# Optimization experiments

Measured on AMD Instinct MI355X. Metric: run time of the kernel, lower is better.

The kernel has to match this reference:

```python
import jax, jax.numpy as jnp
import numpy as np

# tcnn HashGrid config from ntc_conf
L = 16            # n_levels
T = 1 << 15       # 2**log2_hashmap_size entries per level
F = 4             # n_features_per_level
BASE = 16.0       # base_resolution
N_PTS = 1_000_000
PRIMES = jnp.array([1, 2654435761, 805459861], dtype=jnp.uint32)  # tcnn spatial hash primes
OFFS = np.array([[(c >> 2) & 1, (c >> 1) & 1, c & 1] for c in range(8)], dtype=np.uint32)  # 8 cube corners


def hash_encode(x, table):
    """Multi-resolution hash grid encoding. x: [N,3] in [0,1], table: [L,T,F] -> [N, L*F]."""
    N = x.shape[0]
    scales = BASE * (2.0 ** jnp.arange(L, dtype=jnp.float32))        # [L]
    pos = x[:, None, :] * scales[None, :, None]                      # [N,L,3]
    p0 = jnp.floor(pos)
    frac = pos - p0                                                  # trilinear weights source
    p0u = p0.astype(jnp.uint32)
    flat_table = table.reshape(L * T, F)
    level_off = (jnp.arange(L, dtype=jnp.uint32) * jnp.uint32(T))[None, :]  # [1,L]
    acc = jnp.zeros((N, L, F), dtype=table.dtype)
    for c in range(8):  # fixed 8 corners -> keeps peak memory at [N,L,F] per corner
        off = jnp.asarray(OFFS[c])                                   # [3] uint32
        corner = p0u + off                                           # [N,L,3]
        h = corner * PRIMES                                          # uint32 wraparound mul
        idx = (h[..., 0] ^ h[..., 1] ^ h[..., 2]) & jnp.uint32(T - 1)  # [N,L]
        feats = flat_table[(idx + level_off).astype(jnp.int32)]      # gather [N,L,F]
        w = jnp.prod(jnp.where(off.astype(bool), frac, 1.0 - frac), axis=-1)  # [N,L]
        acc = acc + w[..., None] * feats
    return acc.reshape(N, L * F)


def setup_inputs() -> dict:
    key = jax.random.key(0)
    k1, k2, k3, k4, k5 = jax.random.split(key, 5)
    xyz = jax.random.normal(k1, (N_PTS, 3), dtype=jnp.float32)
    xyz_bound_min = -jnp.ones((3,), dtype=jnp.float32)
    xyz_bound_max = jnp.ones((3,), dtype=jnp.float32)
    hash_table = jax.random.normal(k2, (L, T, F), dtype=jnp.float32) * 1e-2  # tcnn-style small init
    w0 = jax.random.normal(k3, (64, 64), dtype=jnp.float32) * (1.0 / 8.0)
    w1 = jax.random.normal(k4, (64, 64), dtype=jnp.float32) * (1.0 / 8.0)
    w2 = jax.random.normal(k5, (64, 8), dtype=jnp.float32) * (1.0 / 8.0)
    return {"xyz": xyz, "xyz_bound_min": xyz_bound_min, "xyz_bound_max": xyz_bound_max,
            "hash_table": hash_table, "w0": w0, "w1": w1, "w2": w2}


def reference(xyz, xyz_bound_min, xyz_bound_max, hash_table, w0, w1, w2):
    contracted = (xyz - xyz_bound_min) / (xyz_bound_max - xyz_bound_min)   # [N,3]
    mask = jnp.all((contracted >= 0.0) & (contracted <= 1.0), axis=1)      # [N]
    # Evaluate on all points (clamped) and mask the writes -- equivalent to the
    # original compaction (contracted[mask]) + scatter-back, jit-friendly shapes.
    xin = jnp.clip(contracted, 0.0, 1.0)
    enc = hash_encode(xin, hash_table)                                     # [N,64]
    h = jax.nn.relu(enc @ w0)
    h = jax.nn.relu(h @ w1)
    resi = h @ w2                                                          # [N,8]
    d_xyz = jnp.where(mask[:, None], resi[:, :3], 0.0)
    ident_rot = jnp.array([1.0, 0.0, 0.0, 0.0], dtype=resi.dtype)
    d_rot = jnp.where(mask[:, None], resi[:, 3:7], ident_rot)
    return mask, d_xyz, d_rot
```

## Files before the change

### kernel.cpp

```cpp
#include <hip/hip_runtime.h>
#include <hip/hip_bf16.h>


#define LVL 16
#define TSZ 32768
#define PR1 2654435761u
#define PR2 805459861u
#define SUBS 16
#define STRIDE (SUBS * 1024)

typedef __attribute__((ext_vector_type(8))) short bf16x8;
typedef __attribute__((ext_vector_type(4))) float f32x4;
typedef __attribute__((ext_vector_type(2))) float f32x2;
typedef __attribute__((ext_vector_type(4))) unsigned short u16x4;
typedef __attribute__((ext_vector_type(2))) unsigned int u32x2;
typedef long long i64;

__device__ __forceinline__ unsigned short f2bf(float f) {
    return __builtin_bit_cast(unsigned short, __float2bfloat16(f));
}

__device__ __forceinline__ unsigned f32x4_to_fp8x4(float f0, float f1, float f2, float f3) {
#if __has_builtin(__builtin_amdgcn_cvt_pk_fp8_f32)
    int u = 0;
    u = __builtin_amdgcn_cvt_pk_fp8_f32(f0, f1, u, false);
    u = __builtin_amdgcn_cvt_pk_fp8_f32(f2, f3, u, true);
    return (unsigned)u;
#else
    float ff[4] = { f0, f1, f2, f3 };
    unsigned u = 0;
    for (int k = 0; k < 4; ++k) {
        const float v = ff[k];
        const unsigned s = v < 0.f ? 1u : 0u;
        float av = fabsf(v);
        unsigned b;
        if (av < 6.103515625e-05f) {
            b = 0u;
        } else if (av < 0.015625f) {
            b = (unsigned)rintf(av * 512.f);
        } else {
            int e; float m = frexpf(av, &e);
            unsigned E = (unsigned)(e - 1 + 7);
            unsigned q = (unsigned)rintf(m * 16.f);
            if (q == 16u) { q = 8u; ++E; }
            b = (E << 3) | (q - 8u);
        }
        u |= ((s << 7) | b) << (8 * k);
    }
    return u;
#endif
}

__device__ __forceinline__ unsigned char f32_to_fp8(float v) {
    return (unsigned char)(f32x4_to_fp8x4(v, v, v, v) & 0xffu);
}

__device__ __forceinline__ void fp8x4_to_2f32x2(unsigned r, f32x2& lo, f32x2& hi) {
#if __has_builtin(__builtin_amdgcn_cvt_pk_f32_fp8)
    lo = __builtin_amdgcn_cvt_pk_f32_fp8((int)r, false);
    hi = __builtin_amdgcn_cvt_pk_f32_fp8((int)r, true);
#else
    float f[4];
#pragma unroll
    for (int k = 0; k < 4; ++k) {
        const unsigned b = (r >> (8 * k)) & 0xffu;
        const unsigned s = b >> 7, em = b & 0x7fu, e = em >> 3, m = em & 7u;
        float v;
        if (e) v = __builtin_bit_cast(float, ((e + 120u) << 23) | (m << 20));
        else   v = (float)m * 0.001953125f;
        f[k] = s ? -v : v;
    }
    lo = (f32x2){ f[0], f[1] };
    hi = (f32x2){ f[2], f[3] };
#endif
}

__global__ __launch_bounds__(1024) void k_enc(
    const float* __restrict__ xyz, const float* __restrict__ bmin, const float* __restrict__ bmax,
    const float* __restrict__ table, float* __restrict__ out,
    unsigned* __restrict__ enc, int N, int Npad,
    const float* __restrict__ w0, const float* __restrict__ w1,
    const float* __restrict__ w2, char* __restrict__ wbase)
{
    __shared__ unsigned tabL[TSZ];

    const int t   = threadIdx.x;
    const int l   = blockIdx.x & 15;
    const int sub = blockIdx.x >> 4;

    {
        const float4* __restrict__ src =
            reinterpret_cast<const float4*>(table + (size_t)l * TSZ * 4);
#pragma unroll 4
        for (int j = 0; j < 32; ++j) {
            const int idx = j * 1024 + t;
            const float4 a = src[idx];
            tabL[idx] = f32x4_to_fp8x4(a.x * 256.f, a.y * 256.f, a.z * 256.f, a.w * 256.f);
        }
    }

    if (blockIdx.x == 16 * SUBS - 1 && t < 256) {
        unsigned char*  wf8 = (unsigned char*)wbase;
        unsigned short* wf1 = (unsigned short*)(wbase + 4096);
        unsigned short* wf2 = (unsigned short*)(wbase + 4096 + 8192);
#pragma unroll
        for (int q = 0; q < 16; ++q) {
            const int s = q * 256 + t;
            const int e = s & 7, f = s >> 3;
            const int ln = f & 63, ntkk = f >> 6;
            const int k = (ntkk & 1) * 32 + (ln >> 4) * 8 + e;
            const int n = (ntkk >> 1) * 16 + (ln & 15);
            wf8[s] = f32_to_fp8(w0[k * 64 + n]);
            wf1[s] = f2bf(w1[k * 64 + n]);
        }
#pragma unroll
        for (int q = 0; q < 4; ++q) {
            const int s = q * 256 + t;
            const int e = s & 7, f = s >> 3;
            const int ln = f & 63, kk = f >> 6;
            const int k = kk * 32 + (ln >> 4) * 8 + e;
            const int n = ln & 15;
            wf2[s] = (n < 8) ? f2bf(w2[k * 8 + n]) : (unsigned short)0;
        }
    }
    __syncthreads();

    const float bx0 = bmin[0], by0 = bmin[1], bz0 = bmin[2];
    const float iex = 1.f / (bmax[0] - bx0);
    const float iey = 1.f / (bmax[1] - by0);
    const float iez = 1.f / (bmax[2] - bz0);
    const float scale = 16.f * (float)(1u << l);
    unsigned* __restrict__ encL = enc + (size_t)l * Npad;
    const bool isL0 = (l == 0);

    const unsigned PR1_4 = PR1 << 2;
    const unsigned PR2_4 = PR2 << 2;
    const unsigned M2 = (TSZ - 1u) << 2;

    int p = sub * 1024 + t;
    if (p < Npad) {
        int pc = p < N ? p : N - 1;
        float cxr = xyz[3 * pc + 0], cyr = xyz[3 * pc + 1], czr = xyz[3 * pc + 2];

        for (; p < Npad; ) {
            const int pn  = p + STRIDE;
            const int pnc = (pn < N) ? pn : (N - 1);
            const float nxr = xyz[3 * pnc + 0];
            const float nyr = xyz[3 * pnc + 1];
            const float nzr = xyz[3 * pnc + 2];

            const float ccx = (cxr - bx0) * iex;
            const float ccy = (cyr - by0) * iey;
            const float ccz = (czr - bz0) * iez;
            if (isL0 && p < N) {
                const bool inside = (ccx >= 0.f) && (ccx <= 1.f) && (ccy >= 0.f) &&
                                    (ccy <= 1.f) && (ccz >= 0.f) && (ccz <= 1.f);
                out[p] = inside ? 1.f : 0.f;
            }
            const float x = fminf(fmaxf(ccx, 0.f), 1.f);
            const float y = fminf(fmaxf(ccy, 0.f), 1.f);
            const float z = fminf(fmaxf(ccz, 0.f), 1.f);

            const float px = x * scale, py = y * scale, pz = z * scale;
            const float fx = floorf(px), fy = floorf(py), fz = floorf(pz);
            const float rx = px - fx, ry = py - fy, rz = pz - fz;
            const unsigned ux = (unsigned)fx, uy = (unsigned)fy, uz = (unsigned)fz;

            const unsigned ux4 = ux << 2;
            const unsigned hy4 = uy * PR1_4, hz4 = uz * PR2_4;
            const unsigned hxy2[4] = {
                (ux4        ^ hy4)           & M2,
                (ux4        ^ (hy4 + PR1_4)) & M2,
                ((ux4 + 4u) ^ hy4)           & M2,
                ((ux4 + 4u) ^ (hy4 + PR1_4)) & M2 };
            const unsigned hz2[2] = { hz4 & M2, (hz4 + PR2_4) & M2 };

            const float wx0 = 1.f - rx, wy0 = 1.f - ry, wz0 = 1.f - rz;
            const f32x2 wyp = { wy0, ry };
            const f32x2 wxyA = (f32x2){ wx0, wx0 } * wyp;
            const f32x2 wxyB = (f32x2){ rx,  rx  } * wyp;
            const f32x2 wz2 = { wz0, rz };
            const f32x2 w8[4] = {
                (f32x2){ wxyA[0], wxyA[0] } * wz2,
                (f32x2){ wxyA[1], wxyA[1] } * wz2,
                (f32x2){ wxyB[0], wxyB[0] } * wz2,
                (f32x2){ wxyB[1], wxyB[1] } * wz2 };

            unsigned r[8];
#pragma unroll
            for (int c = 0; c < 8; ++c)
                r[c] = *reinterpret_cast<const unsigned*>(
                    reinterpret_cast<const char*>(tabL) + (hxy2[c >> 1] ^ hz2[c & 1]));

            f32x2 a01 = { 0.f, 0.f }, a23 = { 0.f, 0.f };
#pragma unroll
            for (int c = 0; c < 8; ++c) {
                f32x2 lo, hi;
                fp8x4_to_2f32x2(r[c], lo, hi);
                const float w = w8[c >> 1][c & 1];
                const f32x2 w2 = { w, w };
                a01 += w2 * lo;
                a23 += w2 * hi;
            }

            const unsigned v = f32x4_to_fp8x4(a01[0], a01[1], a23[0], a23[1]);
            __builtin_nontemporal_store(v, encL + p);

            p = pn; cxr = nxr; cyr = nyr; czr = nzr;
        }
    }
}

__global__ __launch_bounds__(256) void k_mlp(
    const char* __restrict__ wbase, const unsigned* __restrict__ enc,
    float* __restrict__ out, int N, int Npad)
{
    __shared__ unsigned short hT[8 * 256 * 8];
    __shared__ float resS[256 * 8];

    const unsigned char*  wf8 = (const unsigned char*)wbase;
    const unsigned short* wf1 = (const unsigned short*)(wbase + 4096);
    const unsigned short* wf2 = (const unsigned short*)(wbase + 4096 + 8192);

    const int t = threadIdx.x, wv = t >> 6, ln = t & 63;
    const int col = ln & 15, g = ln >> 4;
    const int ptb = blockIdx.x * 256;
    const int i = ptb + t;

    u32x2 a0[2][4];
#pragma unroll
    for (int kk = 0; kk < 2; ++kk)
#pragma unroll
        for (int mt = 0; mt < 4; ++mt) {
            const size_t pt = (size_t)ptb + wv * 64 + mt * 16 + col;
            const int j = kk * 4 + g;
            u32x2 a;
            a[0] = __builtin_nontemporal_load(enc + (size_t)(2 * j)     * Npad + pt);
            a[1] = __builtin_nontemporal_load(enc + (size_t)(2 * j + 1) * Npad + pt);
            a0[kk][mt] = a;
        }
    u32x2 b0[4][2];
#pragma unroll
    for (int nt = 0; nt < 4; ++nt)
#pragma unroll
        for (int kk = 0; kk < 2; ++kk)
            b0[nt][kk] = *reinterpret_cast<const u32x2*>(wf8 + ((nt * 2 + kk) * 64 + ln) * 8);

    f32x4 acc[4][4];
#pragma unroll
    for (int mt = 0; mt < 4; ++mt)
#pragma unroll
        for (int nt = 0; nt < 4; ++nt) acc[mt][nt] = (f32x4){0.f, 0.f, 0.f, 0.f};

#pragma unroll
    for (int kk = 0; kk < 2; ++kk)
#pragma unroll
        for (int nt = 0; nt < 4; ++nt)
#pragma unroll
            for (int mt = 0; mt < 4; ++mt)
                acc[mt][nt] = __builtin_amdgcn_mfma_f32_16x16x32_fp8_fp8(
                    __builtin_bit_cast(i64, a0[kk][mt]),
                    __builtin_bit_cast(i64, b0[nt][kk]), acc[mt][nt], 0, 0, 0);

#pragma unroll
    for (int mt = 0; mt < 4; ++mt)
#pragma unroll
        for (int nt = 0; nt < 4; ++nt) {
            const int kt = nt * 2 + (col >> 3), j = col & 7;
#pragma unroll
            for (int r = 0; r < 4; ++r)
                hT[kt * 2048 + (wv * 64 + mt * 16 + g * 4 + r) * 8 + j] =
                    f2bf(fmaxf(acc[mt][nt][r], 0.f) * 0.00390625f);
        }

    bf16x8 b1[4][2];
#pragma unroll
    for (int nt = 0; nt < 4; ++nt)
#pragma unroll
        for (int kk = 0; kk < 2; ++kk)
            b1[nt][kk] = *reinterpret_cast<const bf16x8*>(wf1 + ((nt * 2 + kk) * 64 + ln) * 8);

#pragma unroll
    for (int mt = 0; mt < 4; ++mt)
#pragma unroll
        for (int nt = 0; nt < 4; ++nt) acc[mt][nt] = (f32x4){0.f, 0.f, 0.f, 0.f};

#pragma unroll
    for (int kk = 0; kk < 2; ++kk) {
        bf16x8 a[4];
#pragma unroll
        for (int mt = 0; mt < 4; ++mt)
            a[mt] = *reinterpret_cast<bf16x8*>(
                &hT[(kk * 4 + g) * 2048 + (wv * 64 + mt * 16 + col) * 8]);
#pragma unroll
        for (int nt = 0; nt < 4; ++nt)
#pragma unroll
            for (int mt = 0; mt < 4; ++mt)
                acc[mt][nt] = __builtin_amdgcn_mfma_f32_16x16x32_bf16(a[mt], b1[nt][kk], acc[mt][nt], 0, 0, 0);
    }

#pragma unroll
    for (int mt = 0; mt < 4; ++mt)
#pragma unroll
        for (int nt = 0; nt < 4; ++nt) {
            const int kt = nt * 2 + (col >> 3), j = col & 7;
#pragma unroll
            for (int r = 0; r < 4; ++r)
                hT[kt * 2048 + (wv * 64 + mt * 16 + g * 4 + r) * 8 + j] =
                    f2bf(fmaxf(acc[mt][nt][r], 0.f));
        }

    f32x4 acc2[4];
#pragma unroll
    for (int mt = 0; mt < 4; ++mt) acc2[mt] = (f32x4){0.f, 0.f, 0.f, 0.f};

#pragma unroll
    for (int kk = 0; kk < 2; ++kk) {
        const bf16x8 b2 = *reinterpret_cast<const bf16x8*>(wf2 + (kk * 64 + ln) * 8);
        bf16x8 a[4];
#pragma unroll
        for (int mt = 0; mt < 4; ++mt)
            a[mt] = *reinterpret_cast<bf16x8*>(
                &hT[(kk * 4 + g) * 2048 + (wv * 64 + mt * 16 + col) * 8]);
#pragma unroll
        for (int mt = 0; mt < 4; ++mt)
            acc2[mt] = __builtin_amdgcn_mfma_f32_16x16x32_bf16(a[mt], b2, acc2[mt], 0, 0, 0);
    }

    if (col < 8) {
#pragma unroll
        for (int mt = 0; mt < 4; ++mt)
#pragma unroll
            for (int r = 0; r < 4; ++r)
                resS[(wv * 64 + mt * 16 + g * 4 + r) * 8 + col] = acc2[mt][r];
    }
    __syncthreads();

    if (i < N) {
        const bool inside = (out[i] != 0.f);
        const f32x4 lo = *reinterpret_cast<f32x4*>(&resS[t * 8 + 0]);
        const f32x4 hi = *reinterpret_cast<f32x4*>(&resS[t * 8 + 4]);

        float* __restrict__ dxyz = out + N;
        dxyz[3 * i + 0] = inside ? lo.x : 0.f;
        dxyz[3 * i + 1] = inside ? lo.y : 0.f;
        dxyz[3 * i + 2] = inside ? lo.z : 0.f;

        float4* __restrict__ drot = reinterpret_cast<float4*>(out + 4 * (size_t)N);
        drot[i] = inside ? make_float4(lo.w, hi.x, hi.y, hi.z)
                         : make_float4(1.f, 0.f, 0.f, 0.f);
    }
}

__global__ __launch_bounds__(256) void ntc_fused(
    const float* __restrict__ xyz, const float* __restrict__ bmin, const float* __restrict__ bmax,
    const float* __restrict__ table, const float* __restrict__ w0, const float* __restrict__ w1,
    const float* __restrict__ w2, float* __restrict__ out, int N)
{
    __shared__ unsigned short encT[8 * 256 * 8];
    __shared__ unsigned short w0t[64 * 64];
    __shared__ unsigned short w1t[64 * 64];
    __shared__ unsigned short w2t[16 * 64];

    const int t = threadIdx.x, wv = t >> 6, ln = t & 63;
    const int col = ln & 15, g = ln >> 4;

#pragma unroll
    for (int it = 0; it < 16; ++it) {
        const int idx = it * 256 + t;
        const int k = idx >> 6, n = idx & 63;
        w0t[n * 64 + k] = f2bf(w0[idx]);
        w1t[n * 64 + k] = f2bf(w1[idx]);
    }
#pragma unroll
    for (int q = 0; q < 4; ++q) {
        const int idx = t * 4 + q;
        const int n = idx >> 6, k = idx & 63;
        w2t[idx] = (n < 8) ? f2bf(w2[k * 8 + n]) : (unsigned short)0;
    }

    const int i = blockIdx.x * 256 + t;
    const int ic = (i < N) ? i : (N - 1);
    const float bx0 = bmin[0], by0 = bmin[1], bz0 = bmin[2];
    const float ex = bmax[0] - bx0, ey = bmax[1] - by0, ez = bmax[2] - bz0;
    const float cx = (xyz[3 * ic + 0] - bx0) / ex;
    const float cy = (xyz[3 * ic + 1] - by0) / ey;
    const float cz = (xyz[3 * ic + 2] - bz0) / ez;
    const bool inside = (cx >= 0.f) && (cx <= 1.f) && (cy >= 0.f) && (cy <= 1.f) &&
                        (cz >= 0.f) && (cz <= 1.f);
    const float x = fminf(fmaxf(cx, 0.f), 1.f);
    const float y = fminf(fmaxf(cy, 0.f), 1.f);
    const float z = fminf(fmaxf(cz, 0.f), 1.f);
    const float4* __restrict__ tab = reinterpret_cast<const float4*>(table);

    for (int l = 0; l < LVL; ++l) {
        const float scale = 16.f * (float)(1u << l);
        const float px = x * scale, py = y * scale, pz = z * scale;
        const float fx = floorf(px), fy = floorf(py), fz = floorf(pz);
        const float rx = px - fx, ry = py - fy, rz = pz - fz;
        const unsigned ux = (unsigned)fx, uy = (unsigned)fy, uz = (unsigned)fz;
        const unsigned hx[2] = { ux, ux + 1u };
        const unsigned hy[2] = { uy * PR1, (uy + 1u) * PR1 };
        const unsigned hz[2] = { uz * PR2, (uz + 1u) * PR2 };
        const float wx[2] = { 1.f - rx, rx };
        const float wy[2] = { 1.f - ry, ry };
        const float wz[2] = { 1.f - rz, rz };
        float a0 = 0.f, a1 = 0.f, a2 = 0.f, a3 = 0.f;
#pragma unroll
        for (int c = 0; c < 8; ++c) {
            const int ox = (c >> 2) & 1, oy = (c >> 1) & 1, oz = c & 1;
            const unsigned idx = (hx[ox] ^ hy[oy] ^ hz[oz]) & (TSZ - 1u);
            const float4 f4 = tab[l * TSZ + idx];
            const float w = wx[ox] * wy[oy] * wz[oz];
            a0 = fmaf(w, f4.x, a0); a1 = fmaf(w, f4.y, a1);
            a2 = fmaf(w, f4.z, a2); a3 = fmaf(w, f4.w, a3);
        }
        u16x4 v = { f2bf(a0), f2bf(a1), f2bf(a2), f2bf(a3) };
        *reinterpret_cast<u16x4*>(&encT[(l >> 1) * 2048 + t * 8 + (l & 1) * 4]) = v;
    }
    __syncthreads();

    f32x4 acc[4][4];
#pragma unroll
    for (int mt = 0; mt < 4; ++mt)
#pragma unroll
        for (int nt = 0; nt < 4; ++nt) acc[mt][nt] = (f32x4){0.f, 0.f, 0.f, 0.f};
#pragma unroll
    for (int kk = 0; kk < 2; ++kk) {
        bf16x8 a[4];
#pragma unroll
        for (int mt = 0; mt < 4; ++mt)
            a[mt] = *reinterpret_cast<bf16x8*>(&encT[(kk * 4 + g) * 2048 + (wv * 64 + mt * 16 + col) * 8]);
#pragma unroll
        for (int nt = 0; nt < 4; ++nt) {
            bf16x8 b = *reinterpret_cast<bf16x8*>(&w0t[(nt * 16 + col) * 64 + kk * 32 + g * 8]);
#pragma unroll
            for (int mt = 0; mt < 4; ++mt)
                acc[mt][nt] = __builtin_amdgcn_mfma_f32_16x16x32_bf16(a[mt], b, acc[mt][nt], 0, 0, 0);
        }
    }
    __syncthreads();
#pragma unroll
    for (int mt = 0; mt < 4; ++mt)
#pragma unroll
        for (int nt = 0; nt < 4; ++nt) {
            const int kt = nt * 2 + (col >> 3), j = col & 7;
#pragma unroll
            for (int r = 0; r < 4; ++r)
                encT[kt * 2048 + (wv * 64 + mt * 16 + g * 4 + r) * 8 + j] = f2bf(fmaxf(acc[mt][nt][r], 0.f));
        }
    __syncthreads();
#pragma unroll
    for (int mt = 0; mt < 4; ++mt)
#pragma unroll
        for (int nt = 0; nt < 4; ++nt) acc[mt][nt] = (f32x4){0.f, 0.f, 0.f, 0.f};
#pragma unroll
    for (int kk = 0; kk < 2; ++kk) {
        bf16x8 a[4];
#pragma unroll
        for (int mt = 0; mt < 4; ++mt)
            a[mt] = *reinterpret_cast<bf16x8*>(&encT[(kk * 4 + g) * 2048 + (wv * 64 + mt * 16 + col) * 8]);
#pragma unroll
        for (int nt = 0; nt < 4; ++nt) {
            bf16x8 b = *reinterpret_cast<bf16x8*>(&w1t[(nt * 16 + col) * 64 + kk * 32 + g * 8]);
#pragma unroll
            for (int mt = 0; mt < 4; ++mt)
                acc[mt][nt] = __builtin_amdgcn_mfma_f32_16x16x32_bf16(a[mt], b, acc[mt][nt], 0, 0, 0);
        }
    }
    __syncthreads();
#pragma unroll
    for (int mt = 0; mt < 4; ++mt)
#pragma unroll
        for (int nt = 0; nt < 4; ++nt) {
            const int kt = nt * 2 + (col >> 3), j = col & 7;
#pragma unroll
            for (int r = 0; r < 4; ++r)
                encT[kt * 2048 + (wv * 64 + mt * 16 + g * 4 + r) * 8 + j] = f2bf(fmaxf(acc[mt][nt][r], 0.f));
        }
    __syncthreads();
    f32x4 acc2[4];
#pragma unroll
    for (int mt = 0; mt < 4; ++mt) acc2[mt] = (f32x4){0.f, 0.f, 0.f, 0.f};
#pragma unroll
    for (int kk = 0; kk < 2; ++kk) {
        bf16x8 a[4];
#pragma unroll
        for (int mt = 0; mt < 4; ++mt)
            a[mt] = *reinterpret_cast<bf16x8*>(&encT[(kk * 4 + g) * 2048 + (wv * 64 + mt * 16 + col) * 8]);
        bf16x8 b = *reinterpret_cast<bf16x8*>(&w2t[col * 64 + kk * 32 + g * 8]);
#pragma unroll
        for (int mt = 0; mt < 4; ++mt)
            acc2[mt] = __builtin_amdgcn_mfma_f32_16x16x32_bf16(a[mt], b, acc2[mt], 0, 0, 0);
    }
    __syncthreads();
    float* res = reinterpret_cast<float*>(encT);
    if (col < 8) {
#pragma unroll
        for (int mt = 0; mt < 4; ++mt)
#pragma unroll
            for (int r = 0; r < 4; ++r)
                res[(wv * 64 + mt * 16 + g * 4 + r) * 8 + col] = acc2[mt][r];
    }
    __syncthreads();
    if (i < N) {
        const f32x4 lo = *reinterpret_cast<f32x4*>(&res[t * 8 + 0]);
        const f32x4 hi = *reinterpret_cast<f32x4*>(&res[t * 8 + 4]);
        out[i] = inside ? 1.f : 0.f;
        float* __restrict__ dxyz = out + N;
        dxyz[3 * i + 0] = inside ? lo.x : 0.f;
        dxyz[3 * i + 1] = inside ? lo.y : 0.f;
        dxyz[3 * i + 2] = inside ? lo.z : 0.f;
        float4* __restrict__ drot = reinterpret_cast<float4*>(out + 4 * (size_t)N);
        drot[i] = inside ? make_float4(lo.w, hi.x, hi.y, hi.z)
                         : make_float4(1.f, 0.f, 0.f, 0.f);
    }
}

extern "C" void kernel_launch(void* const* d_in, const int* in_sizes, int n_in,
                              void* d_out, int out_size, void* d_ws, size_t ws_size,
                              hipStream_t stream) {
    const float* xyz   = (const float*)d_in[0];
    const float* bmin  = (const float*)d_in[1];
    const float* bmax  = (const float*)d_in[2];
    const float* table = (const float*)d_in[3];
    const float* w0    = (const float*)d_in[4];
    const float* w1    = (const float*)d_in[5];
    const float* w2    = (const float*)d_in[6];
    float* out = (float*)d_out;

    const int N = in_sizes[0] / 3;
    const int nb = (N + 255) / 256;
    const int Npad = nb * 256;

    size_t offEnc = 14336;
    size_t need = offEnc + (size_t)Npad * 64;

    if (ws_size >= need) {
        char* wbase   = (char*)d_ws;
        unsigned* enc = (unsigned*)((char*)d_ws + offEnc);
        k_enc<<<16 * SUBS, 1024, 0, stream>>>(xyz, bmin, bmax, table, out, enc, N, Npad,
                                              w0, w1, w2, wbase);
        k_mlp<<<nb, 256, 0, stream>>>(wbase, enc, out, N, Npad);
    } else {
        ntc_fused<<<nb, 256, 0, stream>>>(xyz, bmin, bmax, table, w0, w1, w2, out, N);
    }
}
```

Measured before the change: 173.4 us.

## Make MLP kernel persistent with next-tile encoding prefetch

The MLP kernel now launches at most 1024 blocks that walk the point tiles with a grid stride. Weight fragments for layers 0 and 2 are loaded once per block instead of once per tile. The next tile's encodings and mask value are loaded into registers while the current tile's MFMA chain runs, to hide global-load latency. The block-wide barrier before the result write-out is dropped because each wave only reads LDS rows it wrote itself. The prefetch adds register pressure, which can lower occupancy.

After: 168.8 us. -2.6%, faster.

```diff
diff --git a/kernel.cpp b/kernel.cpp
--- a/kernel.cpp
+++ b/kernel.cpp
@@ -213,7 +213,7 @@
 
 __global__ __launch_bounds__(256) void k_mlp(
     const char* __restrict__ wbase, const unsigned* __restrict__ enc,
-    float* __restrict__ out, int N, int Npad)
+    float* __restrict__ out, int N, int Npad, int nb)
 {
     __shared__ unsigned short hT[8 * 256 * 8];
     __shared__ float resS[256 * 8];
@@ -224,131 +224,171 @@
 
     const int t = threadIdx.x, wv = t >> 6, ln = t & 63;
     const int col = ln & 15, g = ln >> 4;
-    const int ptb = blockIdx.x * 256;
-    const int i = ptb + t;
-
-    u32x2 a0[2][4];
-#pragma unroll
-    for (int kk = 0; kk < 2; ++kk)
-#pragma unroll
-        for (int mt = 0; mt < 4; ++mt) {
-            const size_t pt = (size_t)ptb + wv * 64 + mt * 16 + col;
-            const int j = kk * 4 + g;
-            u32x2 a;
-            a[0] = __builtin_nontemporal_load(enc + (size_t)(2 * j)     * Npad + pt);
-            a[1] = __builtin_nontemporal_load(enc + (size_t)(2 * j + 1) * Npad + pt);
-            a0[kk][mt] = a;
-        }
+
     u32x2 b0[4][2];
 #pragma unroll
     for (int nt = 0; nt < 4; ++nt)
 #pragma unroll
         for (int kk = 0; kk < 2; ++kk)
             b0[nt][kk] = *reinterpret_cast<const u32x2*>(wf8 + ((nt * 2 + kk) * 64 + ln) * 8);
-
-    f32x4 acc[4][4];
-#pragma unroll
-    for (int mt = 0; mt < 4; ++mt)
-#pragma unroll
-        for (int nt = 0; nt < 4; ++nt) acc[mt][nt] = (f32x4){0.f, 0.f, 0.f, 0.f};
-
+    bf16x8 b2f[2];
 #pragma unroll
     for (int kk = 0; kk < 2; ++kk)
+        b2f[kk] = *reinterpret_cast<const bf16x8*>(wf2 + (kk * 64 + ln) * 8);
+
+    int tile = blockIdx.x;
+    if (tile >= nb) return;
+
+    u32x2 aC[2][4];
+    {
+        const int ptb = tile * 256;
+#pragma unroll
+        for (int kk = 0; kk < 2; ++kk)
+#pragma unroll
+            for (int mt = 0; mt < 4; ++mt) {
+                const size_t pt = (size_t)ptb + wv * 64 + mt * 16 + col;
+                const int j = kk * 4 + g;
+                u32x2 a;
+                a[0] = __builtin_nontemporal_load(enc + (size_t)(2 * j)     * Npad + pt);
+                a[1] = __builtin_nontemporal_load(enc + (size_t)(2 * j + 1) * Npad + pt);
+                aC[kk][mt] = a;
+            }
+    }
+    float mkC = 0.f;
+    { const int i0 = tile * 256 + t; if (i0 < N) mkC = out[i0]; }
+
+    for (;;) {
+        const int tn = tile + (int)gridDim.x;
+        const bool more = (tn < nb);
+
+        u32x2 aN[2][4];
+        float mkN = 0.f;
+        if (more) {
+            const int ptb = tn * 256;
+#pragma unroll
+            for (int kk = 0; kk < 2; ++kk)
+#pragma unroll
+                for (int mt = 0; mt < 4; ++mt) {
+                    const size_t pt = (size_t)ptb + wv * 64 + mt * 16 + col;
+                    const int j = kk * 4 + g;
+                    u32x2 a;
+                    a[0] = __builtin_nontemporal_load(enc + (size_t)(2 * j)     * Npad + pt);
+                    a[1] = __builtin_nontemporal_load(enc + (size_t)(2 * j + 1) * Npad + pt);
+                    aN[kk][mt] = a;
+                }
+            const int i1 = tn * 256 + t; if (i1 < N) mkN = out[i1];
+        }
+        bf16x8 b1[4][2];
 #pragma unroll
         for (int nt = 0; nt < 4; ++nt)
 #pragma unroll
+            for (int kk = 0; kk < 2; ++kk)
+                b1[nt][kk] = *reinterpret_cast<const bf16x8*>(wf1 + ((nt * 2 + kk) * 64 + ln) * 8);
+
+        f32x4 acc[4][4];
+#pragma unroll
+        for (int mt = 0; mt < 4; ++mt)
+#pragma unroll
+            for (int nt = 0; nt < 4; ++nt) acc[mt][nt] = (f32x4){0.f, 0.f, 0.f, 0.f};
+
+#pragma unroll
+        for (int kk = 0; kk < 2; ++kk)
+#pragma unroll
+            for (int nt = 0; nt < 4; ++nt)
+#pragma unroll
+                for (int mt = 0; mt < 4; ++mt)
+                    acc[mt][nt] = __builtin_amdgcn_mfma_f32_16x16x32_fp8_fp8(
+                        __builtin_bit_cast(i64, aC[kk][mt]),
+                        __builtin_bit_cast(i64, b0[nt][kk]), acc[mt][nt], 0, 0, 0);
+
+#pragma unroll
+        for (int mt = 0; mt < 4; ++mt)
+#pragma unroll
+            for (int nt = 0; nt < 4; ++nt) {
+                const int kt = nt * 2 + (col >> 3), j = col & 7;
+#pragma unroll
+                for (int r = 0; r < 4; ++r)
+                    hT[kt * 2048 + (wv * 64 + mt * 16 + g * 4 + r) * 8 + j] =
+                        f2bf(fmaxf(acc[mt][nt][r], 0.f) * 0.00390625f);
+            }
+
+#pragma unroll
+        for (int mt = 0; mt < 4; ++mt)
+#pragma unroll
+            for (int nt = 0; nt < 4; ++nt) acc[mt][nt] = (f32x4){0.f, 0.f, 0.f, 0.f};
+
+#pragma unroll
+        for (int kk = 0; kk < 2; ++kk) {
+            bf16x8 a[4];
+#pragma unroll
             for (int mt = 0; mt < 4; ++mt)
-                acc[mt][nt] = __builtin_amdgcn_mfma_f32_16x16x32_fp8_fp8(
-                    __builtin_bit_cast(i64, a0[kk][mt]),
-                    __builtin_bit_cast(i64, b0[nt][kk]), acc[mt][nt], 0, 0, 0);
-
-#pragma unroll
-    for (int mt = 0; mt < 4; ++mt)
-#pragma unroll
-        for (int nt = 0; nt < 4; ++nt) {
-            const int kt = nt * 2 + (col >> 3), j = col & 7;
-#pragma unroll
-            for (int r = 0; r < 4; ++r)
-                hT[kt * 2048 + (wv * 64 + mt * 16 + g * 4 + r) * 8 + j] =
-                    f2bf(fmaxf(acc[mt][nt][r], 0.f) * 0.00390625f);
-        }
-
-    bf16x8 b1[4][2];
-#pragma unroll
-    for (int nt = 0; nt < 4; ++nt)
+                a[mt] = *reinterpret_cast<bf16x8*>(
+                    &hT[(kk * 4 + g) * 2048 + (wv * 64 + mt * 16 + col) * 8]);
+#pragma unroll
+            for (int nt = 0; nt < 4; ++nt)
+#pragma unroll
+                for (int mt = 0; mt < 4; ++mt)
+                    acc[mt][nt] = __builtin_amdgcn_mfma_f32_16x16x32_bf16(a[mt], b1[nt][kk], acc[mt][nt], 0, 0, 0);
+        }
+
+#pragma unroll
+        for (int mt = 0; mt < 4; ++mt)
+#pragma unroll
+            for (int nt = 0; nt < 4; ++nt) {
+                const int kt = nt * 2 + (col >> 3), j = col & 7;
+#pragma unroll
+                for (int r = 0; r < 4; ++r)
+                    hT[kt * 2048 + (wv * 64 + mt * 16 + g * 4 + r) * 8 + j] =
+                        f2bf(fmaxf(acc[mt][nt][r], 0.f));
+            }
+
+        f32x4 acc2[4];
+#pragma unroll
+        for (int mt = 0; mt < 4; ++mt) acc2[mt] = (f32x4){0.f, 0.f, 0.f, 0.f};
+
+#pragma unroll
+        for (int kk = 0; kk < 2; ++kk) {
+            bf16x8 a[4];
+#pragma unroll
+            for (int mt = 0; mt < 4; ++mt)
+                a[mt] = *reinterpret_cast<bf16x8*>(
+                    &hT[(kk * 4 + g) * 2048 + (wv * 64 + mt * 16 + col) * 8]);
+#pragma unroll
+            for (int mt = 0; mt < 4; ++mt)
+                acc2[mt] = __builtin_amdgcn_mfma_f32_16x16x32_bf16(a[mt], b2f[kk], acc2[mt], 0, 0, 0);
+        }
+
+        if (col < 8) {
+#pragma unroll
+            for (int mt = 0; mt < 4; ++mt)
+#pragma unroll
+                for (int r = 0; r < 4; ++r)
+                    resS[(wv * 64 + mt * 16 + g * 4 + r) * 8 + col] = acc2[mt][r];
+        }
+
+        const int i = tile * 256 + t;
+        if (i < N) {
+            const bool inside = (mkC != 0.f);
+            const f32x4 lo = *reinterpret_cast<f32x4*>(&resS[t * 8 + 0]);
+            const f32x4 hi = *reinterpret_cast<f32x4*>(&resS[t * 8 + 4]);
+
+            float* __restrict__ dxyz = out + N;
+            dxyz[3 * i + 0] = inside ? lo.x : 0.f;
+            dxyz[3 * i + 1] = inside ? lo.y : 0.f;
+            dxyz[3 * i + 2] = inside ? lo.z : 0.f;
+
+            float4* __restrict__ drot = reinterpret_cast<float4*>(out + 4 * (size_t)N);
+            drot[i] = inside ? make_float4(lo.w, hi.x, hi.y, hi.z)
+                             : make_float4(1.f, 0.f, 0.f, 0.f);
+        }
+
+        if (!more) break;
 #pragma unroll
         for (int kk = 0; kk < 2; ++kk)
-            b1[nt][kk] = *reinterpret_cast<const bf16x8*>(wf1 + ((nt * 2 + kk) * 64 + ln) * 8);
-
-#pragma unroll
-    for (int mt = 0; mt < 4; ++mt)
-#pragma unroll
-        for (int nt = 0; nt < 4; ++nt) acc[mt][nt] = (f32x4){0.f, 0.f, 0.f, 0.f};
-
-#pragma unroll
-    for (int kk = 0; kk < 2; ++kk) {
-        bf16x8 a[4];
-#pragma unroll
-        for (int mt = 0; mt < 4; ++mt)
-            a[mt] = *reinterpret_cast<bf16x8*>(
-                &hT[(kk * 4 + g) * 2048 + (wv * 64 + mt * 16 + col) * 8]);
-#pragma unroll
-        for (int nt = 0; nt < 4; ++nt)
-#pragma unroll
-            for (int mt = 0; mt < 4; ++mt)
-                acc[mt][nt] = __builtin_amdgcn_mfma_f32_16x16x32_bf16(a[mt], b1[nt][kk], acc[mt][nt], 0, 0, 0);
-    }
-
-#pragma unroll
-    for (int mt = 0; mt < 4; ++mt)
-#pragma unroll
-        for (int nt = 0; nt < 4; ++nt) {
-            const int kt = nt * 2 + (col >> 3), j = col & 7;
-#pragma unroll
-            for (int r = 0; r < 4; ++r)
-                hT[kt * 2048 + (wv * 64 + mt * 16 + g * 4 + r) * 8 + j] =
-                    f2bf(fmaxf(acc[mt][nt][r], 0.f));
-        }
-
-    f32x4 acc2[4];
-#pragma unroll
-    for (int mt = 0; mt < 4; ++mt) acc2[mt] = (f32x4){0.f, 0.f, 0.f, 0.f};
-
-#pragma unroll
-    for (int kk = 0; kk < 2; ++kk) {
-        const bf16x8 b2 = *reinterpret_cast<const bf16x8*>(wf2 + (kk * 64 + ln) * 8);
-        bf16x8 a[4];
-#pragma unroll
-        for (int mt = 0; mt < 4; ++mt)
-            a[mt] = *reinterpret_cast<bf16x8*>(
-                &hT[(kk * 4 + g) * 2048 + (wv * 64 + mt * 16 + col) * 8]);
-#pragma unroll
-        for (int mt = 0; mt < 4; ++mt)
-            acc2[mt] = __builtin_amdgcn_mfma_f32_16x16x32_bf16(a[mt], b2, acc2[mt], 0, 0, 0);
-    }
-
-    if (col < 8) {
-#pragma unroll
-        for (int mt = 0; mt < 4; ++mt)
-#pragma unroll
-            for (int r = 0; r < 4; ++r)
-                resS[(wv * 64 + mt * 16 + g * 4 + r) * 8 + col] = acc2[mt][r];
-    }
-    __syncthreads();
-
-    if (i < N) {
-        const bool inside = (out[i] != 0.f);
-        const f32x4 lo = *reinterpret_cast<f32x4*>(&resS[t * 8 + 0]);
-        const f32x4 hi = *reinterpret_cast<f32x4*>(&resS[t * 8 + 4]);
-
-        float* __restrict__ dxyz = out + N;
-        dxyz[3 * i + 0] = inside ? lo.x : 0.f;
-        dxyz[3 * i + 1] = inside ? lo.y : 0.f;
-        dxyz[3 * i + 2] = inside ? lo.z : 0.f;
-
-        float4* __restrict__ drot = reinterpret_cast<float4*>(out + 4 * (size_t)N);
-        drot[i] = inside ? make_float4(lo.w, hi.x, hi.y, hi.z)
-                         : make_float4(1.f, 0.f, 0.f, 0.f);
+#pragma unroll
+            for (int mt = 0; mt < 4; ++mt) aC[kk][mt] = aN[kk][mt];
+        mkC = mkN;
+        tile = tn;
     }
 }
 
@@ -539,9 +579,10 @@
     if (ws_size >= need) {
         char* wbase   = (char*)d_ws;
         unsigned* enc = (unsigned*)((char*)d_ws + offEnc);
+        const int nbK = nb < 1024 ? nb : 1024;
         k_enc<<<16 * SUBS, 1024, 0, stream>>>(xyz, bmin, bmax, table, out, enc, N, Npad,
                                               w0, w1, w2, wbase);
-        k_mlp<<<nb, 256, 0, stream>>>(wbase, enc, out, N, Npad);
+        k_mlp<<<nbK, 256, 0, stream>>>(wbase, enc, out, N, Npad, nb);
     } else {
         ntc_fused<<<nb, 256, 0, stream>>>(xyz, bmin, bmax, table, w0, w1, w2, out, N);
     }
```
